# Optimization experiments

Hardware: AMD Instinct MI355X
Metric: run time of the kernel (lower is better)

## Reference

```python
import jax, jax.numpy as jnp
import numpy as np

ALPHA = 0.2  # LeakyReLU negative slope
NEG_INF = -9e15

def setup_inputs() -> dict:
    key = jax.random.key(0)
    k1, k2, k3, k4, k5 = jax.random.split(key, 5)
    B, N, Fin, Fout = 8, 2048, 128, 128
    h = jax.random.normal(k1, (B, N, Fin), dtype=jnp.float32)
    adj = jax.random.randint(k2, (N, N), 0, 2, dtype=jnp.int32)
    dist = jax.random.uniform(k3, (N, N), dtype=jnp.float32)
    W = jax.random.normal(k4, (Fin, Fout), dtype=jnp.float32) * (1.414 * (6.0 / (Fin + Fout)) ** 0.5)
    a = jax.random.normal(k5, (2 * Fout, 1), dtype=jnp.float32) * 0.1
    distance_scaler = jnp.ones((1,), dtype=jnp.float32)
    return {"h": h, "adj": adj, "dist": dist, "W": W, "a": a, "distance_scaler": distance_scaler}

def reference(h, adj, dist, W, a, distance_scaler):
    # h: [B,N,Fin], adj/dist: [N,N], W: [Fin,Fout], a: [2*Fout,1]
    h_prime = jnp.einsum('bnf,fh->bnh', h, W)              # [B,N,Fout]
    Fout = h_prime.shape[-1]
    a1, a2 = a[:Fout, 0], a[Fout:, 0]
    # additive score: a1.h_i + a2.h_j, equivalent to cat([h_i,h_j]) @ a
    si = h_prime @ a1                                      # [B,N]
    sj = h_prime @ a2                                      # [B,N]
    e = jax.nn.leaky_relu(si[:, :, None] + sj[:, None, :], negative_slope=ALPHA)  # [B,N,N]
    dist_bias = -jnp.log(dist + 1e-6) * distance_scaler[0]  # [N,N]
    scores = e + dist_bias[None, :, :]
    scores = jnp.where(adj[None, :, :] > 0, scores, NEG_INF)
    attention = jax.nn.softmax(scores, axis=2)             # [B,N,N]
    # dropout=identity in eval mode
    out = jnp.einsum('bij,bjh->bih', attention, h_prime)   # [B,N,Fout]
    return jax.nn.elu(out)
```

## Files before the change

kernel.cpp:

```cpp
#include <hip/hip_runtime.h>
#include <hip/hip_bf16.h>

typedef __attribute__((ext_vector_type(4))) float f32x4;
typedef __attribute__((ext_vector_type(8))) short short8;
typedef __attribute__((ext_vector_type(4))) unsigned short ushort4v;
typedef _Float16 f16x8 __attribute__((ext_vector_type(8)));

#define NB 8
#define NN 2048
#define NF 128
#define LOG2E 1.4426950408889634f
#define MASK_NEG_H -60000.0f

static __device__ __forceinline__ unsigned short f2bf(float f) {
    union { __hip_bfloat16 b; unsigned short u; } cv;
    cv.b = __float2bfloat16(f);
    return cv.u;
}

__global__ __launch_bounds__(256) void k_pre(
    const float* __restrict__ h, const int* __restrict__ adj,
    const float* __restrict__ dist, const float* __restrict__ W,
    const float* __restrict__ a, const float* __restrict__ scaler,
    unsigned short* __restrict__ vfrag, float* __restrict__ siC,
    float* __restrict__ sjC, _Float16* __restrict__ biasF)
{
    __shared__ __align__(16) unsigned char smem[34816];
    const int bid = blockIdx.x;
    const int t = threadIdx.x;

    if (bid < 256) {
        unsigned char* WT = smem;
        float* wa1 = (float*)(smem + 32768);
        float* wa2 = wa1 + NF;

        const int lane = t & 63;
        const int w = t >> 6;
        const int b = bid >> 5;
        const int i0 = (bid & 31) << 6;

        {
            const int f = t >> 1;
            const int c0 = (t & 1) << 6;
            float s1 = 0.f, s2 = 0.f;
            const float* wrow = W + f * NF + c0;
            const float* a1p = a + c0;
            const float* a2p = a + NF + c0;
            #pragma unroll 8
            for (int c = 0; c < 64; ++c) {
                float wv = wrow[c];
                s1 += wv * a1p[c];
                s2 += wv * a2p[c];
                int col = c0 + c;
                int dst = col * 256 + ((2 * f) ^ ((col & 15) << 4));
                *reinterpret_cast<unsigned short*>(&WT[dst]) = f2bf(wv);
            }
            s1 += __shfl_xor(s1, 1);
            s2 += __shfl_xor(s2, 1);
            if ((t & 1) == 0) { wa1[f] = s1 * LOG2E; wa2[f] = s2 * LOG2E; }
        }
        __syncthreads();

        const int l15 = lane & 15;
        const int arow = i0 + w * 16 + l15;
        const int kofs = (lane >> 4) << 3;
        const float* hrow = h + (size_t)(b * NN + arow) * NF + kofs;
        const int swz = l15 << 4;

        f32x4 acc[8];
        #pragma unroll
        for (int nt = 0; nt < 8; ++nt) acc[nt] = (f32x4)(0.f);
        float s1 = 0.f, s2 = 0.f;

        #pragma unroll
        for (int k0 = 0; k0 < NF; k0 += 32) {
            f32x4 h0 = *reinterpret_cast<const f32x4*>(hrow + k0);
            f32x4 h1 = *reinterpret_cast<const f32x4*>(hrow + k0 + 4);
            f32x4 w1lo = *reinterpret_cast<const f32x4*>(&wa1[k0 + kofs]);
            f32x4 w1hi = *reinterpret_cast<const f32x4*>(&wa1[k0 + kofs + 4]);
            f32x4 w2lo = *reinterpret_cast<const f32x4*>(&wa2[k0 + kofs]);
            f32x4 w2hi = *reinterpret_cast<const f32x4*>(&wa2[k0 + kofs + 4]);
            short8 af;
            #pragma unroll
            for (int e = 0; e < 4; ++e) {
                s1 += h0[e] * w1lo[e] + h1[e] * w1hi[e];
                s2 += h0[e] * w2lo[e] + h1[e] * w2hi[e];
                af[e]     = (short)f2bf(h0[e]);
                af[4 + e] = (short)f2bf(h1[e]);
            }
            const int ib = (2 * (k0 + kofs)) ^ swz;
            #pragma unroll
            for (int nt = 0; nt < 8; ++nt) {
                short8 bf8 = *reinterpret_cast<short8*>(&WT[(nt * 16 + l15) * 256 + ib]);
                acc[nt] = __builtin_amdgcn_mfma_f32_16x16x32_bf16(af, bf8, acc[nt], 0, 0, 0);
            }
        }

        s1 += __shfl_xor(s1, 16); s1 += __shfl_xor(s1, 32);
        s2 += __shfl_xor(s2, 16); s2 += __shfl_xor(s2, 32);
        if (lane < 16) {
            siC[b * NN + arow] = s1;
            sjC[b * NN + arow] = s2;
        }

        const int J0 = i0 + w * 16 + ((lane >> 4) << 2);
        const int s = J0 >> 5;
        const int jq = (J0 >> 3) & 3;
        const int eh = J0 & 7;
        #pragma unroll
        for (int nt = 0; nt < 8; ++nt) {
            ushort4v pk;
            #pragma unroll
            for (int e = 0; e < 4; ++e) pk[e] = f2bf(acc[nt][e]);
            *reinterpret_cast<ushort4v*>(
                vfrag + (((size_t)(b * 64 + s) * 8 + nt) * 64 + (l15 | (jq << 4))) * 8 + eh) = pk;
        }
    } else {
        _Float16 (*st)[64][8] = (_Float16 (*)[64][8])smem;
        const int bid2 = bid - 256;
        const int iblk = bid2 >> 3;
        const int jch = bid2 & 7;
        const int i_l = t >> 4;
        const int o2 = t & 15;
        const int i = iblk * 16 + i_l;
        const int jbase = jch * 256 + o2 * 16;
        const float sc = scaler[0];

        const int* ap = adj + (size_t)i * NN + jbase;
        const float* dp = dist + (size_t)i * NN + jbase;
        int av[16]; float dv[16];
        *reinterpret_cast<int4*>(&av[0])  = *reinterpret_cast<const int4*>(ap);
        *reinterpret_cast<int4*>(&av[4])  = *reinterpret_cast<const int4*>(ap + 4);
        *reinterpret_cast<int4*>(&av[8])  = *reinterpret_cast<const int4*>(ap + 8);
        *reinterpret_cast<int4*>(&av[12]) = *reinterpret_cast<const int4*>(ap + 12);
        *reinterpret_cast<float4*>(&dv[0])  = *reinterpret_cast<const float4*>(dp);
        *reinterpret_cast<float4*>(&dv[4])  = *reinterpret_cast<const float4*>(dp + 4);
        *reinterpret_cast<float4*>(&dv[8])  = *reinterpret_cast<const float4*>(dp + 8);
        *reinterpret_cast<float4*>(&dv[12]) = *reinterpret_cast<const float4*>(dp + 12);

        #pragma unroll
        for (int u = 0; u < 2; ++u) {
            const int sl = (o2 * 2 + u) >> 2;
            const int jq = (o2 * 2 + u) & 3;
            f16x8 pk;
            #pragma unroll
            for (int e = 0; e < 8; ++e) {
                const int idx = u * 8 + e;
                float v = (av[idx] > 0) ? (-__log2f(dv[idx] + 1e-6f) * sc) : MASK_NEG_H;
                pk[e] = (_Float16)v;
            }
            *reinterpret_cast<f16x8*>(&st[sl][i_l | (jq << 4)][0]) = pk;
        }
        __syncthreads();

        const int w = t >> 6, lane = t & 63;
        #pragma unroll
        for (int sub = 0; sub < 2; ++sub) {
            const int fs = w * 2 + sub;
            *reinterpret_cast<f16x8*>(
                biasF + ((size_t)(iblk * 64 + jch * 8 + fs) * 64 + lane) * 8) =
                *reinterpret_cast<f16x8*>(&st[fs][lane][0]);
        }
    }
}

__global__ __launch_bounds__(512, 4) void k_attn(
    const unsigned short* __restrict__ vfrag, const float* __restrict__ siC,
    const float* __restrict__ sjC, const _Float16* __restrict__ biasF,
    float* __restrict__ out)
{
    __shared__ __align__(16) float red[4][8][64][4];
    __shared__ float lp[2][4][16];

    const int t = threadIdx.x;
    const int lane = t & 63;
    const int w = t >> 6;
    const int rt = w & 3;
    const int jh = w >> 2;
    const int l15 = lane & 15;
    const int hi = lane >> 4;

    const int b = blockIdx.x & 7;
    const int rg = blockIdx.x >> 3;

    const int rowbase = rg * 64 + rt * 16;
    const float si0 = siC[b * NN + rowbase + l15];

    const float* sjp = sjC + b * NN + jh * 1024 + hi * 8;
    const _Float16* bp = biasF +
        ((size_t)((rg * 4 + rt) * 64 + jh * 32) * 64 + lane) * 8;
    const unsigned short* vp = vfrag +
        ((size_t)(b * 64 + jh * 32) * 8) * 512 + lane * 8;

    f32x4 acc[8];
    #pragma unroll
    for (int ct = 0; ct < 8; ++ct) acc[ct] = (f32x4)(0.f);
    float ls0 = 0.f;

    #pragma unroll 2
    for (int sl = 0; sl < 32; ++sl) {
        f32x4 sj0 = *reinterpret_cast<const f32x4*>(sjp + sl * 32);
        f32x4 sj1 = *reinterpret_cast<const f32x4*>(sjp + sl * 32 + 4);
        f16x8 bv = *reinterpret_cast<const f16x8*>(bp + sl * 512);
        short8 pa;
        #pragma unroll
        for (int e = 0; e < 8; ++e) {
            const float sjv = (e < 4) ? sj0[e] : sj1[e - 4];
            float x = si0 + sjv;
            x = fmaxf(x, 0.2f * x) + (float)bv[e];
            float p = __builtin_amdgcn_exp2f(x);
            ls0 += p;
            pa[e] = (short)f2bf(p);
        }
        const unsigned short* vs = vp + sl * 4096;
        #pragma unroll
        for (int ct = 0; ct < 8; ++ct) {
            const short8 bfr = *reinterpret_cast<const short8*>(vs + ct * 512);
            acc[ct] = __builtin_amdgcn_mfma_f32_16x16x32_bf16(pa, bfr, acc[ct], 0, 0, 0);
        }
    }

    ls0 += __shfl_xor(ls0, 16);
    ls0 += __shfl_xor(ls0, 32);
    if (lane < 16) lp[jh][rt][l15] = ls0;

    if (jh == 1) {
        #pragma unroll
        for (int ct = 0; ct < 8; ++ct)
            *reinterpret_cast<f32x4*>(&red[rt][ct][lane][0]) = acc[ct];
    }
    __syncthreads();
    if (jh == 0) {
        float linv[4];
        #pragma unroll
        for (int e = 0; e < 4; ++e) {
            const int rr = (hi << 2) + e;
            linv[e] = 1.0f / (lp[0][rt][rr] + lp[1][rt][rr]);
        }
        #pragma unroll
        for (int ct = 0; ct < 8; ++ct) {
            f32x4 o = acc[ct] + *reinterpret_cast<const f32x4*>(&red[rt][ct][lane][0]);
            const int col = ct * 16 + l15;
            #pragma unroll
            for (int e = 0; e < 4; ++e) {
                const int row = rowbase + (hi << 2) + e;
                float v = o[e] * linv[e];
                v = (v > 0.f) ? v : expm1f(v);
                out[(size_t)(b * NN + row) * NF + col] = v;
            }
        }
    }
}

extern "C" void kernel_launch(void* const* d_in, const int* in_sizes, int n_in,
                              void* d_out, int out_size, void* d_ws, size_t ws_size,
                              hipStream_t stream) {
    (void)in_sizes; (void)n_in; (void)out_size; (void)ws_size;
    const float* h      = (const float*)d_in[0];
    const int*   adj    = (const int*)d_in[1];
    const float* dist   = (const float*)d_in[2];
    const float* W      = (const float*)d_in[3];
    const float* a      = (const float*)d_in[4];
    const float* scaler = (const float*)d_in[5];
    float* out = (float*)d_out;

    char* ws = (char*)d_ws;
    unsigned short* vfrag = (unsigned short*)ws;
    float* siC      = (float*)(ws + 4 * 1024 * 1024);
    float* sjC      = (float*)(ws + 4 * 1024 * 1024 + 65536);
    _Float16* biasF = (_Float16*)(ws + 4 * 1024 * 1024 + 2 * 65536);

    k_pre<<<dim3(1280), dim3(256), 0, stream>>>(h, adj, dist, W, a, scaler,
                                                vfrag, siC, sjC, biasF);
    k_attn<<<dim3(NB * NN / 64), dim3(512), 0, stream>>>(vfrag, siC, sjC, biasF, out);
}
```

Baseline: 46.76 us.

## Split attention key dimension across eight waves with two row tiles each

Reorganizes k_attn so each block handles 32 rows instead of 64. Each of 8 waves now covers a quarter-length key slice and computes two 16-row tiles, so every V fragment load feeds two MFMAs. Partial accumulators are combined through a multi-stage shared-memory tree reduction with several extra barriers, and the grid doubles. The aim is better V reuse per load and more parallelism per block. The cost is higher register pressure from 16 accumulators and more reduction and synchronisation overhead.

```diff
diff --git a/kernel.cpp b/kernel.cpp
--- a/kernel.cpp
+++ b/kernel.cpp
@@ -169,87 +169,117 @@
     const float* __restrict__ sjC, const _Float16* __restrict__ biasF,
     float* __restrict__ out)
 {
-    __shared__ __align__(16) float red[4][8][64][4];
-    __shared__ float lp[2][4][16];
+    __shared__ __align__(16) f32x4 red[4][1024];
+    __shared__ float lp[8][2][16];
 
     const int t = threadIdx.x;
     const int lane = t & 63;
-    const int w = t >> 6;
-    const int rt = w & 3;
-    const int jh = w >> 2;
+    const int jq = t >> 6;
     const int l15 = lane & 15;
     const int hi = lane >> 4;
 
     const int b = blockIdx.x & 7;
     const int rg = blockIdx.x >> 3;
 
-    const int rowbase = rg * 64 + rt * 16;
+    const int rowbase = rg * 32;
     const float si0 = siC[b * NN + rowbase + l15];
-
-    const float* sjp = sjC + b * NN + jh * 1024 + hi * 8;
-    const _Float16* bp = biasF +
-        ((size_t)((rg * 4 + rt) * 64 + jh * 32) * 64 + lane) * 8;
+    const float si1 = siC[b * NN + rowbase + 16 + l15];
+
+    const float* sjp = sjC + b * NN + jq * 256 + hi * 8;
+    const _Float16* bp0 = biasF + ((size_t)(rg * 2 * 64 + jq * 8) * 64 + lane) * 8;
+    const _Float16* bp1 = bp0 + 32768;
     const unsigned short* vp = vfrag +
-        ((size_t)(b * 64 + jh * 32) * 8) * 512 + lane * 8;
-
-    f32x4 acc[8];
+        ((size_t)(b * 64 + jq * 8) * 8) * 512 + lane * 8;
+
+    f32x4 acc[2][8];
     #pragma unroll
-    for (int ct = 0; ct < 8; ++ct) acc[ct] = (f32x4)(0.f);
-    float ls0 = 0.f;
+    for (int rs = 0; rs < 2; ++rs)
+        #pragma unroll
+        for (int ct = 0; ct < 8; ++ct) acc[rs][ct] = (f32x4)(0.f);
+    float ls0 = 0.f, ls1 = 0.f;
 
     #pragma unroll 2
-    for (int sl = 0; sl < 32; ++sl) {
+    for (int sl = 0; sl < 8; ++sl) {
         f32x4 sj0 = *reinterpret_cast<const f32x4*>(sjp + sl * 32);
         f32x4 sj1 = *reinterpret_cast<const f32x4*>(sjp + sl * 32 + 4);
-        f16x8 bv = *reinterpret_cast<const f16x8*>(bp + sl * 512);
-        short8 pa;
+        f16x8 bv0 = *reinterpret_cast<const f16x8*>(bp0 + sl * 512);
+        f16x8 bv1 = *reinterpret_cast<const f16x8*>(bp1 + sl * 512);
+        short8 pa0, pa1;
         #pragma unroll
         for (int e = 0; e < 8; ++e) {
             const float sjv = (e < 4) ? sj0[e] : sj1[e - 4];
-            float x = si0 + sjv;
-            x = fmaxf(x, 0.2f * x) + (float)bv[e];
-            float p = __builtin_amdgcn_exp2f(x);
-            ls0 += p;
-            pa[e] = (short)f2bf(p);
+            float x0 = si0 + sjv;
+            x0 = fmaxf(x0, 0.2f * x0) + (float)bv0[e];
+            float p0 = __builtin_amdgcn_exp2f(x0);
+            ls0 += p0;
+            pa0[e] = (short)f2bf(p0);
+            float x1 = si1 + sjv;
+            x1 = fmaxf(x1, 0.2f * x1) + (float)bv1[e];
+            float p1 = __builtin_amdgcn_exp2f(x1);
+            ls1 += p1;
+            pa1[e] = (short)f2bf(p1);
         }
         const unsigned short* vs = vp + sl * 4096;
         #pragma unroll
         for (int ct = 0; ct < 8; ++ct) {
             const short8 bfr = *reinterpret_cast<const short8*>(vs + ct * 512);
-            acc[ct] = __builtin_amdgcn_mfma_f32_16x16x32_bf16(pa, bfr, acc[ct], 0, 0, 0);
+            acc[0][ct] = __builtin_amdgcn_mfma_f32_16x16x32_bf16(pa0, bfr, acc[0][ct], 0, 0, 0);
+            acc[1][ct] = __builtin_amdgcn_mfma_f32_16x16x32_bf16(pa1, bfr, acc[1][ct], 0, 0, 0);
         }
     }
 
-    ls0 += __shfl_xor(ls0, 16);
-    ls0 += __shfl_xor(ls0, 32);
-    if (lane < 16) lp[jh][rt][l15] = ls0;
-
-    if (jh == 1) {
-        #pragma unroll
-        for (int ct = 0; ct < 8; ++ct)
-            *reinterpret_cast<f32x4*>(&red[rt][ct][lane][0]) = acc[ct];
-    }
-    __syncthreads();
-    if (jh == 0) {
-        float linv[4];
+    ls0 += __shfl_xor(ls0, 16); ls0 += __shfl_xor(ls0, 32);
+    ls1 += __shfl_xor(ls1, 16); ls1 += __shfl_xor(ls1, 32);
+    if (lane < 16) { lp[jq][0][l15] = ls0; lp[jq][1][l15] = ls1; }
+
+    #define WACC(buf) { _Pragma("unroll") for (int rs = 0; rs < 2; ++rs)      \
+        _Pragma("unroll") for (int ct = 0; ct < 8; ++ct)                      \
+        red[buf][(rs * 8 + ct) * 64 + lane] = acc[rs][ct]; }
+    #define AACC(buf) { _Pragma("unroll") for (int rs = 0; rs < 2; ++rs)      \
+        _Pragma("unroll") for (int ct = 0; ct < 8; ++ct)                      \
+        acc[rs][ct] += red[buf][(rs * 8 + ct) * 64 + lane]; }
+
+    if (jq & 1) WACC(jq >> 1)
+    __syncthreads();
+    if (!(jq & 1)) AACC(jq >> 1)
+    __syncthreads();
+    if (jq == 2) WACC(0)
+    if (jq == 6) WACC(1)
+    __syncthreads();
+    if (jq == 0) AACC(0)
+    if (jq == 4) AACC(1)
+    __syncthreads();
+    if (jq == 4) WACC(0)
+    __syncthreads();
+    if (jq == 0) {
+        AACC(0)
+        float linv0[4], linv1[4];
         #pragma unroll
         for (int e = 0; e < 4; ++e) {
             const int rr = (hi << 2) + e;
-            linv[e] = 1.0f / (lp[0][rt][rr] + lp[1][rt][rr]);
+            float t0 = 0.f, t1 = 0.f;
+            #pragma unroll
+            for (int q = 0; q < 8; ++q) { t0 += lp[q][0][rr]; t1 += lp[q][1][rr]; }
+            linv0[e] = 1.0f / t0;
+            linv1[e] = 1.0f / t1;
         }
         #pragma unroll
         for (int ct = 0; ct < 8; ++ct) {
-            f32x4 o = acc[ct] + *reinterpret_cast<const f32x4*>(&red[rt][ct][lane][0]);
             const int col = ct * 16 + l15;
             #pragma unroll
             for (int e = 0; e < 4; ++e) {
-                const int row = rowbase + (hi << 2) + e;
-                float v = o[e] * linv[e];
-                v = (v > 0.f) ? v : expm1f(v);
-                out[(size_t)(b * NN + row) * NF + col] = v;
+                const int r0 = rowbase + (hi << 2) + e;
+                float v0 = acc[0][ct][e] * linv0[e];
+                v0 = (v0 > 0.f) ? v0 : expm1f(v0);
+                out[(size_t)(b * NN + r0) * NF + col] = v0;
+                float v1 = acc[1][ct][e] * linv1[e];
+                v1 = (v1 > 0.f) ? v1 : expm1f(v1);
+                out[(size_t)(b * NN + r0 + 16) * NF + col] = v1;
             }
         }
     }
+    #undef WACC
+    #undef AACC
 }
 
 extern "C" void kernel_launch(void* const* d_in, const int* in_sizes, int n_in,
@@ -272,5 +302,5 @@
 
     k_pre<<<dim3(1280), dim3(256), 0, stream>>>(h, adj, dist, W, a, scaler,
                                                 vfrag, siC, sjC, biasF);
-    k_attn<<<dim3(NB * NN / 64), dim3(512), 0, stream>>>(vfrag, siC, sjC, biasF, out);
+    k_attn<<<dim3(NB * NN / 32), dim3(512), 0, stream>>>(vfrag, siC, sjC, biasF, out);
 }
```

Measured after the change: 55.73 us. 19.2% more time.

## Stage V fragments in double-buffered LDS shared across row-tile waves

Applied to the files above, without the earlier changes.

Previously each of the four row-tile waves loaded V fragments directly from global memory, so every fragment was fetched four times per block. The attention kernel now cooperatively loads 32 KB V tiles into a double-buffered LDS region and prefetches the next tile into registers while the MFMAs consume the current one. The two j-halves are interleaved per tile instead of split into contiguous ranges, and the reduction buffer reuses the same LDS. This adds 64 KB of LDS and a block-wide barrier per tile, which may reduce occupancy below the four blocks per CU requested by the launch bounds.

```diff
diff --git a/kernel.cpp b/kernel.cpp
--- a/kernel.cpp
+++ b/kernel.cpp
@@ -169,7 +169,7 @@
     const float* __restrict__ sjC, const _Float16* __restrict__ biasF,
     float* __restrict__ out)
 {
-    __shared__ __align__(16) float red[4][8][64][4];
+    __shared__ __align__(16) unsigned char vt[2][32768];
     __shared__ float lp[2][4][16];
 
     const int t = threadIdx.x;
@@ -186,38 +186,71 @@
     const int rowbase = rg * 64 + rt * 16;
     const float si0 = siC[b * NN + rowbase + l15];
 
-    const float* sjp = sjC + b * NN + jh * 1024 + hi * 8;
-    const _Float16* bp = biasF +
-        ((size_t)((rg * 4 + rt) * 64 + jh * 32) * 64 + lane) * 8;
-    const unsigned short* vp = vfrag +
-        ((size_t)(b * 64 + jh * 32) * 8) * 512 + lane * 8;
+    const unsigned short* vsrc = vfrag + (size_t)b * 64 * 4096 + t * 8;
+    const int dofs = t * 16;
+
+    const _Float16* bp = biasF + ((size_t)((rg * 4 + rt) * 64) * 64 + lane) * 8;
+    const float* sjb = sjC + b * NN + hi * 8;
 
     f32x4 acc[8];
     #pragma unroll
     for (int ct = 0; ct < 8; ++ct) acc[ct] = (f32x4)(0.f);
     float ls0 = 0.f;
 
-    #pragma unroll 2
-    for (int sl = 0; sl < 32; ++sl) {
-        f32x4 sj0 = *reinterpret_cast<const f32x4*>(sjp + sl * 32);
-        f32x4 sj1 = *reinterpret_cast<const f32x4*>(sjp + sl * 32 + 4);
-        f16x8 bv = *reinterpret_cast<const f16x8*>(bp + sl * 512);
-        short8 pa;
-        #pragma unroll
-        for (int e = 0; e < 8; ++e) {
-            const float sjv = (e < 4) ? sj0[e] : sj1[e - 4];
-            float x = si0 + sjv;
-            x = fmaxf(x, 0.2f * x) + (float)bv[e];
-            float p = __builtin_amdgcn_exp2f(x);
-            ls0 += p;
-            pa[e] = (short)f2bf(p);
-        }
-        const unsigned short* vs = vp + sl * 4096;
-        #pragma unroll
-        for (int ct = 0; ct < 8; ++ct) {
-            const short8 bfr = *reinterpret_cast<const short8*>(vs + ct * 512);
-            acc[ct] = __builtin_amdgcn_mfma_f32_16x16x32_bf16(pa, bfr, acc[ct], 0, 0, 0);
-        }
+    {
+        short8 v0 = *reinterpret_cast<const short8*>(vsrc);
+        short8 v1 = *reinterpret_cast<const short8*>(vsrc + 4096);
+        short8 v2 = *reinterpret_cast<const short8*>(vsrc + 8192);
+        short8 v3 = *reinterpret_cast<const short8*>(vsrc + 12288);
+        *reinterpret_cast<short8*>(&vt[0][dofs])         = v0;
+        *reinterpret_cast<short8*>(&vt[0][dofs + 8192])  = v1;
+        *reinterpret_cast<short8*>(&vt[0][dofs + 16384]) = v2;
+        *reinterpret_cast<short8*>(&vt[0][dofs + 24576]) = v3;
+    }
+    __syncthreads();
+
+    for (int tl = 0; tl < 16; ++tl) {
+        const int cur = tl & 1;
+        short8 v0, v1, v2, v3;
+        if (tl < 15) {
+            const unsigned short* ns = vsrc + (tl + 1) * 16384;
+            v0 = *reinterpret_cast<const short8*>(ns);
+            v1 = *reinterpret_cast<const short8*>(ns + 4096);
+            v2 = *reinterpret_cast<const short8*>(ns + 8192);
+            v3 = *reinterpret_cast<const short8*>(ns + 12288);
+        }
+        #pragma unroll
+        for (int q = 0; q < 2; ++q) {
+            const int s = tl * 4 + jh * 2 + q;
+            f32x4 sj0 = *reinterpret_cast<const f32x4*>(sjb + s * 32);
+            f32x4 sj1 = *reinterpret_cast<const f32x4*>(sjb + s * 32 + 4);
+            f16x8 bv = *reinterpret_cast<const f16x8*>(bp + s * 512);
+            short8 pa;
+            #pragma unroll
+            for (int e = 0; e < 8; ++e) {
+                const float sjv = (e < 4) ? sj0[e] : sj1[e - 4];
+                float x = si0 + sjv;
+                x = fmaxf(x, 0.2f * x) + (float)bv[e];
+                float p = __builtin_amdgcn_exp2f(x);
+                ls0 += p;
+                pa[e] = (short)f2bf(p);
+            }
+            const int lsl = jh * 2 + q;
+            #pragma unroll
+            for (int ct = 0; ct < 8; ++ct) {
+                const short8 bfr = *reinterpret_cast<const short8*>(
+                    &vt[cur][(lsl * 8 + ct) * 1024 + lane * 16]);
+                acc[ct] = __builtin_amdgcn_mfma_f32_16x16x32_bf16(pa, bfr, acc[ct], 0, 0, 0);
+            }
+        }
+        if (tl < 15) {
+            unsigned char* db = &vt[cur ^ 1][dofs];
+            *reinterpret_cast<short8*>(db)          = v0;
+            *reinterpret_cast<short8*>(db + 8192)   = v1;
+            *reinterpret_cast<short8*>(db + 16384)  = v2;
+            *reinterpret_cast<short8*>(db + 24576)  = v3;
+        }
+        __syncthreads();
     }
 
     ls0 += __shfl_xor(ls0, 16);
@@ -227,7 +260,7 @@
     if (jh == 1) {
         #pragma unroll
         for (int ct = 0; ct < 8; ++ct)
-            *reinterpret_cast<f32x4*>(&red[rt][ct][lane][0]) = acc[ct];
+            *reinterpret_cast<f32x4*>(&vt[0][(rt * 8 + ct) * 1024 + lane * 16]) = acc[ct];
     }
     __syncthreads();
     if (jh == 0) {
@@ -239,7 +272,8 @@
         }
         #pragma unroll
         for (int ct = 0; ct < 8; ++ct) {
-            f32x4 o = acc[ct] + *reinterpret_cast<const f32x4*>(&red[rt][ct][lane][0]);
+            f32x4 o = acc[ct] + *reinterpret_cast<const f32x4*>(
+                &vt[0][(rt * 8 + ct) * 1024 + lane * 16]);
             const int col = ct * 16 + l15;
             #pragma unroll
             for (int e = 0; e < 4; ++e) {
```

After: 52.47 us. 1.12x slower.

## Split key range four ways per block and double-buffer V fragments in registers

Applied to the files above, without the earlier changes.

Each attention block now covers 32 rows instead of 64, with four waves splitting the 2048 keys for each 16-row tile instead of two. This doubles the grid size. The inner loop prefetches the next step's V fragments into a second register buffer so global loads overlap the exp and MFMA work. The cross-wave accumulator reduction becomes a multi-stage LDS tree with extra barriers, and the extra V buffer raises register pressure, which may limit occupancy.

```diff
diff --git a/kernel.cpp b/kernel.cpp
--- a/kernel.cpp
+++ b/kernel.cpp
@@ -169,87 +169,118 @@
     const float* __restrict__ sjC, const _Float16* __restrict__ biasF,
     float* __restrict__ out)
 {
-    __shared__ __align__(16) float red[4][8][64][4];
-    __shared__ float lp[2][4][16];
+    __shared__ __align__(16) f32x4 red[4][512];
+    __shared__ float lp[4][2][16];
 
     const int t = threadIdx.x;
     const int lane = t & 63;
     const int w = t >> 6;
-    const int rt = w & 3;
-    const int jh = w >> 2;
+    const int rt = w & 1;
+    const int jh = w >> 1;
     const int l15 = lane & 15;
     const int hi = lane >> 4;
 
     const int b = blockIdx.x & 7;
     const int rg = blockIdx.x >> 3;
 
-    const int rowbase = rg * 64 + rt * 16;
+    const int rowbase = rg * 32 + rt * 16;
     const float si0 = siC[b * NN + rowbase + l15];
 
-    const float* sjp = sjC + b * NN + jh * 1024 + hi * 8;
+    const float* sjp = sjC + b * NN + jh * 512 + hi * 8;
     const _Float16* bp = biasF +
-        ((size_t)((rg * 4 + rt) * 64 + jh * 32) * 64 + lane) * 8;
+        ((size_t)((rg * 2 + rt) * 64 + jh * 16) * 64 + lane) * 8;
     const unsigned short* vp = vfrag +
-        ((size_t)(b * 64 + jh * 32) * 8) * 512 + lane * 8;
+        ((size_t)(b * 64 + jh * 16) * 8) * 512 + lane * 8;
 
     f32x4 acc[8];
     #pragma unroll
     for (int ct = 0; ct < 8; ++ct) acc[ct] = (f32x4)(0.f);
     float ls0 = 0.f;
 
-    #pragma unroll 2
-    for (int sl = 0; sl < 32; ++sl) {
-        f32x4 sj0 = *reinterpret_cast<const f32x4*>(sjp + sl * 32);
-        f32x4 sj1 = *reinterpret_cast<const f32x4*>(sjp + sl * 32 + 4);
-        f16x8 bv = *reinterpret_cast<const f16x8*>(bp + sl * 512);
-        short8 pa;
-        #pragma unroll
-        for (int e = 0; e < 8; ++e) {
-            const float sjv = (e < 4) ? sj0[e] : sj1[e - 4];
-            float x = si0 + sjv;
-            x = fmaxf(x, 0.2f * x) + (float)bv[e];
-            float p = __builtin_amdgcn_exp2f(x);
-            ls0 += p;
-            pa[e] = (short)f2bf(p);
-        }
-        const unsigned short* vs = vp + sl * 4096;
-        #pragma unroll
-        for (int ct = 0; ct < 8; ++ct) {
-            const short8 bfr = *reinterpret_cast<const short8*>(vs + ct * 512);
-            acc[ct] = __builtin_amdgcn_mfma_f32_16x16x32_bf16(pa, bfr, acc[ct], 0, 0, 0);
-        }
+    short8 va[8], vb[8];
+    #pragma unroll
+    for (int ct = 0; ct < 8; ++ct)
+        va[ct] = *reinterpret_cast<const short8*>(vp + ct * 512);
+
+#define SCORE_MFMA(S, VBUF)                                                    \
+    {                                                                          \
+        f32x4 sj0 = *reinterpret_cast<const f32x4*>(sjp + (S) * 32);           \
+        f32x4 sj1 = *reinterpret_cast<const f32x4*>(sjp + (S) * 32 + 4);       \
+        f16x8 bv = *reinterpret_cast<const f16x8*>(bp + (S) * 512);            \
+        short8 pa;                                                             \
+        _Pragma("unroll")                                                      \
+        for (int e = 0; e < 8; ++e) {                                          \
+            const float sjv = (e < 4) ? sj0[e] : sj1[e - 4];                   \
+            float x = si0 + sjv;                                               \
+            x = fmaxf(x, 0.2f * x) + (float)bv[e];                             \
+            float p = __builtin_amdgcn_exp2f(x);                               \
+            ls0 += p;                                                          \
+            pa[e] = (short)f2bf(p);                                            \
+        }                                                                      \
+        _Pragma("unroll")                                                      \
+        for (int ct = 0; ct < 8; ++ct)                                         \
+            acc[ct] = __builtin_amdgcn_mfma_f32_16x16x32_bf16(                 \
+                pa, VBUF[ct], acc[ct], 0, 0, 0);                               \
     }
+
+    for (int sl = 0; sl < 16; sl += 2) {
+        {
+            const unsigned short* vn = vp + (sl + 1) * 4096;
+            #pragma unroll
+            for (int ct = 0; ct < 8; ++ct)
+                vb[ct] = *reinterpret_cast<const short8*>(vn + ct * 512);
+        }
+        SCORE_MFMA(sl, va)
+        if (sl + 2 < 16) {
+            const unsigned short* vn = vp + (sl + 2) * 4096;
+            #pragma unroll
+            for (int ct = 0; ct < 8; ++ct)
+                va[ct] = *reinterpret_cast<const short8*>(vn + ct * 512);
+        }
+        SCORE_MFMA(sl + 1, vb)
+    }
+#undef SCORE_MFMA
 
     ls0 += __shfl_xor(ls0, 16);
     ls0 += __shfl_xor(ls0, 32);
     if (lane < 16) lp[jh][rt][l15] = ls0;
 
-    if (jh == 1) {
-        #pragma unroll
-        for (int ct = 0; ct < 8; ++ct)
-            *reinterpret_cast<f32x4*>(&red[rt][ct][lane][0]) = acc[ct];
-    }
+#define WACC(buf) { _Pragma("unroll") for (int ct = 0; ct < 8; ++ct)       \
+        red[buf][ct * 64 + lane] = acc[ct]; }
+#define AACC(buf) { _Pragma("unroll") for (int ct = 0; ct < 8; ++ct)       \
+        acc[ct] += red[buf][ct * 64 + lane]; }
+
+    if (jh == 1) WACC(rt * 2)
+    if (jh == 3) WACC(rt * 2 + 1)
+    __syncthreads();
+    if (jh == 0) AACC(rt * 2)
+    if (jh == 2) AACC(rt * 2 + 1)
+    __syncthreads();
+    if (jh == 2) WACC(rt * 2)
     __syncthreads();
     if (jh == 0) {
+        AACC(rt * 2)
         float linv[4];
         #pragma unroll
         for (int e = 0; e < 4; ++e) {
             const int rr = (hi << 2) + e;
-            linv[e] = 1.0f / (lp[0][rt][rr] + lp[1][rt][rr]);
+            linv[e] = 1.0f / (lp[0][rt][rr] + lp[1][rt][rr]
+                            + lp[2][rt][rr] + lp[3][rt][rr]);
         }
         #pragma unroll
         for (int ct = 0; ct < 8; ++ct) {
-            f32x4 o = acc[ct] + *reinterpret_cast<const f32x4*>(&red[rt][ct][lane][0]);
             const int col = ct * 16 + l15;
             #pragma unroll
             for (int e = 0; e < 4; ++e) {
                 const int row = rowbase + (hi << 2) + e;
-                float v = o[e] * linv[e];
+                float v = acc[ct][e] * linv[e];
                 v = (v > 0.f) ? v : expm1f(v);
                 out[(size_t)(b * NN + row) * NF + col] = v;
             }
         }
     }
+#undef WACC
+#undef AACC
 }
 
 extern "C" void kernel_launch(void* const* d_in, const int* in_sizes, int n_in,
@@ -272,5 +303,5 @@
 
     k_pre<<<dim3(1280), dim3(256), 0, stream>>>(h, adj, dist, W, a, scaler,
                                                 vfrag, siC, sjC, biasF);
-    k_attn<<<dim3(NB * NN / 64), dim3(512), 0, stream>>>(vfrag, siC, sjC, biasF, out);
+    k_attn<<<dim3(NB * NN / 32), dim3(512), 0, stream>>>(vfrag, siC, sjC, biasF, out);
 }
```

New measurement: 48.42 us. 1.04x slower.
